# Performance work log

Hardware: AMD Instinct MI355X
Metric: run time of the kernel (lower is better)

Reference implementation:

```python
import jax, jax.numpy as jnp
import numpy as np

B, N, D, H = 2, 2048, 384, 8
Dh = D // H          # 48
G = Dh // 3          # 16 3-vectors per head
EPS = 1e-5


def setup_inputs() -> dict:
    key = jax.random.key(0)
    ks = jax.random.split(key, 8)
    x = jax.random.normal(ks[0], (B, N, D), dtype=jnp.float32)
    # per-node SE(3) frames: proper rotation matrices via QR of random Gaussians
    raw = jax.random.normal(ks[1], (B, N, 3, 3), dtype=jnp.float32)
    q, r = jnp.linalg.qr(raw)
    sign = jnp.sign(jnp.diagonal(r, axis1=-2, axis2=-1))
    frames = q * sign[..., None, :]
    s = 1.0 / np.sqrt(D)
    Wq = jax.random.normal(ks[2], (D, D), dtype=jnp.float32) * s
    Wk = jax.random.normal(ks[3], (D, D), dtype=jnp.float32) * s
    Wv = jax.random.normal(ks[4], (D, D), dtype=jnp.float32) * s
    Wo = jax.random.normal(ks[5], (D, D), dtype=jnp.float32) * s
    bo = jnp.zeros((D,), dtype=jnp.float32)
    gamma = jnp.ones((D,), dtype=jnp.float32)
    beta = jnp.zeros((D,), dtype=jnp.float32)
    return {"x": x, "frames": frames, "Wq": Wq, "Wk": Wk, "Wv": Wv,
            "Wo": Wo, "bo": bo, "gamma": gamma, "beta": beta}


def _rotate(frames, t):
    # t: [B,N,H,Dh] -> rotate each 3-vector chunk by the node's frame R_i
    b, n, h, dh = t.shape
    t3 = t.reshape(b, n, h, dh // 3, 3)
    r3 = jnp.einsum('bnij,bnhgj->bnhgi', frames, t3)
    return r3.reshape(b, n, h, dh)


def reference(x, frames, Wq, Wk, Wv, Wo, bo, gamma, beta):
    b, n, d = x.shape
    Q = (x @ Wq.T).reshape(b, n, H, Dh)
    K = (x @ Wk.T).reshape(b, n, H, Dh)
    V = (x @ Wv.T).reshape(b, n, H, Dh)
    # SE(3) frame-conditioned attention: rotate Q,K into each node's local frame
    Qr = _rotate(frames, Q)
    Kr = _rotate(frames, K)
    scores = jnp.einsum('bqhd,bkhd->bhqk', Qr, Kr) / np.sqrt(Dh)
    attn = jax.nn.softmax(scores, axis=-1)
    out = jnp.einsum('bhqk,bkhd->bqhd', attn, V).reshape(b, n, d)
    out = out @ Wo.T + bo          # out_proj; dropout is identity in eval
    y = x + out                     # residual
    mu = jnp.mean(y, axis=-1, keepdims=True)
    var = jnp.var(y, axis=-1, keepdims=True)
    return (y - mu) * jax.lax.rsqrt(var + EPS) * gamma + beta
```

## Files before the change

### kernel.cpp

```cpp
#include <hip/hip_runtime.h>
#include <hip/hip_bf16.h>
#include <math.h>

constexpr int B = 2, N = 2048, D = 384, H = 8, Dh = 48;
constexpr int M = B * N;
constexpr float EPS = 1e-5f;
constexpr int WSZ = 384 * 384;

typedef short bf16x8 __attribute__((ext_vector_type(8)));
typedef float f32x4 __attribute__((ext_vector_type(4)));

#if __has_builtin(__builtin_amdgcn_exp2f)
#define EXP2(x) __builtin_amdgcn_exp2f(x)
#else
#define EXP2(x) exp2f(x)
#endif

__device__ __forceinline__ ushort f2bf(float f) {
  union { float f; uint u; } v; v.f = f;
  uint r = v.u + 0x7fffu + ((v.u >> 16) & 1u);
  return (ushort)(r >> 16);
}
__device__ __forceinline__ float bf2f(ushort u) {
  union { uint u; float f; } v; v.u = ((uint)u) << 16;
  return v.f;
}
__device__ __forceinline__ uint pk_bf16(float lo, float hi) {
  union { __hip_bfloat162 h; uint u; } v;
  v.h = __float22bfloat162_rn(make_float2(lo, hi));
  return v.u;
}

__device__ __forceinline__ void gload16(const void* g, void* lds) {
  __builtin_amdgcn_global_load_lds(
      (const __attribute__((address_space(1))) unsigned int*)g,
      (__attribute__((address_space(3))) unsigned int*)lds, 16, 0, 0);
}

__global__ __launch_bounds__(256) void pack_all(
    const float* __restrict__ x, const float* __restrict__ Wq,
    const float* __restrict__ Wk, const float* __restrict__ Wv,
    const float* __restrict__ Wo, ushort* __restrict__ xbf,
    ushort* __restrict__ Wqkv, ushort* __restrict__ Wobf) {
  constexpr int XSZ = M * 384;
  int i = (blockIdx.x * 256 + threadIdx.x) * 8;
  const float* src; ushort* dst; int off;
  if (i < XSZ) { src = x; dst = xbf; off = i; }
  else {
    int j = i - XSZ;
    if (j < WSZ)          { src = Wq; dst = Wqkv;           off = j; }
    else if (j < 2 * WSZ) { src = Wk; dst = Wqkv + WSZ;     off = j - WSZ; }
    else if (j < 3 * WSZ) { src = Wv; dst = Wqkv + 2 * WSZ; off = j - 2 * WSZ; }
    else                  { src = Wo; dst = Wobf;           off = j - 3 * WSZ; }
  }
  float4 a = *(const float4*)(src + off);
  float4 b = *(const float4*)(src + off + 4);
  uint4 o;
  o.x = pk_bf16(a.x, a.y);
  o.y = pk_bf16(a.z, a.w);
  o.z = pk_bf16(b.x, b.y);
  o.w = pk_bf16(b.z, b.w);
  *(uint4*)(dst + off) = o;
}

__global__ __launch_bounds__(256) void gemm_qkv(
    const ushort* __restrict__ Abf, const ushort* __restrict__ Wbf,
    ushort* __restrict__ Qpad, ushort* __restrict__ Kpad,
    ushort* __restrict__ Vt) {
  __shared__ ushort Asm[64 * 32];
  __shared__ ushort Bsm[128 * 32];
  const int tid = threadIdx.x, w = tid >> 6, lane = tid & 63;
  const int lq = lane & 15, g = lane >> 4;
  const int brow = blockIdx.y * 64, bcol = blockIdx.x * 128;
  const int wr0 = (w >> 1) * 32, wc0 = (w & 1) * 64;
  const int srow = lane >> 2, scol = (lane & 3) * 8;
  f32x4 acc[2][4];
#pragma unroll
  for (int mi = 0; mi < 2; ++mi)
#pragma unroll
    for (int ni = 0; ni < 4; ++ni) acc[mi][ni] = f32x4{0.f, 0.f, 0.f, 0.f};

  for (int kt = 0; kt < 384; kt += 32) {
    __syncthreads();
    gload16(Abf + (size_t)(brow + w * 16 + srow) * 384 + kt + scol, Asm + w * 512);
#pragma unroll
    for (int i = 0; i < 2; ++i) {
      int seg = w * 2 + i;
      gload16(Wbf + (size_t)(bcol + seg * 16 + srow) * 384 + kt + scol, Bsm + seg * 512);
    }
    __syncthreads();
    bf16x8 a[2], b[4];
#pragma unroll
    for (int mi = 0; mi < 2; ++mi)
      a[mi] = *(const bf16x8*)(Asm + (wr0 + mi * 16 + lq) * 32 + g * 8);
#pragma unroll
    for (int ni = 0; ni < 4; ++ni)
      b[ni] = *(const bf16x8*)(Bsm + (wc0 + ni * 16 + lq) * 32 + g * 8);
#pragma unroll
    for (int mi = 0; mi < 2; ++mi)
#pragma unroll
      for (int ni = 0; ni < 4; ++ni)
        acc[mi][ni] = __builtin_amdgcn_mfma_f32_16x16x32_bf16(a[mi], b[ni], acc[mi][ni], 0, 0, 0);
  }

  if (bcol < 768) {
#pragma unroll
    for (int mi = 0; mi < 2; ++mi)
#pragma unroll
      for (int ni = 0; ni < 4; ++ni) {
        int colD = bcol + wc0 + ni * 16 + lq;
        ushort* dstm = (colD < 384) ? Qpad : Kpad;
        int c = (colD < 384) ? colD : colD - 384;
        int hh = c / 48, dh = c - hh * 48;
#pragma unroll
        for (int r = 0; r < 4; ++r) {
          int row = brow + wr0 + mi * 16 + g * 4 + r;
          dstm[(size_t)row * 512 + hh * 64 + dh] = f2bf(acc[mi][ni][r]);
        }
      }
  } else {
#pragma unroll
    for (int mi = 0; mi < 2; ++mi)
#pragma unroll
      for (int ni = 0; ni < 4; ++ni) {
        int vcol = bcol + wc0 + ni * 16 + lq - 768;
        int hh = vcol / 48, dh = vcol - hh * 48;
#pragma unroll
        for (int r = 0; r < 4; ++r) {
          int row = brow + wr0 + mi * 16 + g * 4 + r;
          int bb = row >> 11, nn = row & 2047;
          Vt[((size_t)(bb * H + hh) * 48 + dh) * N + nn] = f2bf(acc[mi][ni][r]);
        }
      }
  }
}

__global__ __launch_bounds__(256) void rotate_both(
    ushort* __restrict__ Q, ushort* __restrict__ K,
    const float* __restrict__ F, float qscale) {
  constexpr int TOT = M * H * 16;
  int idx = blockIdx.x * 256 + threadIdx.x;
  ushort* T = (idx < TOT) ? Q : K;
  float scale = (idx < TOT) ? qscale : 1.0f;
  int rem = (idx < TOT) ? idx : idx - TOT;
  int gq = rem & 15;
  int nh = rem >> 4;
  int h = nh & 7;
  int bn = nh >> 3;
  ushort* p = T + (size_t)bn * 512 + h * 64;
  if (gq < 8) *(uint*)(p + 48 + gq * 2) = 0u;
  ushort* s = p + gq * 3;
  const float* R = F + (size_t)bn * 9;
  float v0 = bf2f(s[0]), v1 = bf2f(s[1]), v2 = bf2f(s[2]);
  float w0 = (R[0] * v0 + R[1] * v1 + R[2] * v2) * scale;
  float w1 = (R[3] * v0 + R[4] * v1 + R[5] * v2) * scale;
  float w2 = (R[6] * v0 + R[7] * v1 + R[8] * v2) * scale;
  s[0] = f2bf(w0); s[1] = f2bf(w1); s[2] = f2bf(w2);
}

__global__ __launch_bounds__(128) void attn_mfma(
    const ushort* __restrict__ Qpad, const ushort* __restrict__ Kpad,
    const ushort* __restrict__ Vt, ushort* __restrict__ Pacc,
    float* __restrict__ Pml) {
  __shared__ __align__(16) ushort SH[14336];
  ushort* K0 = SH;
  ushort* K1 = SH + 4096;
  ushort* V0 = SH + 8192;
  ushort* V1 = SH + 11264;

  const int bid = blockIdx.x;
  const int wg = (bid & 7) * 128 + (bid >> 3);
  const int qt = wg & 31;
  const int rest = wg >> 5;
  const int h = rest & 7;
  const int b = (rest >> 3) & 1;
  const int half = rest >> 4;
  const int kt0 = half * 1024;
  const int tid = threadIdx.x;
  const int w = tid >> 6;
  const int lane = tid & 63;
  const int lq = lane & 15;
  const int g = lane >> 4;
  const int l7 = lq & 7;
  const int srow8 = lane >> 3;
  const int c8 = (lane & 7) ^ srow8;

  bf16x8 qf[2][2];
  {
    const ushort* qb = Qpad + ((size_t)(b * N) + qt * 64 + w * 32) * 512 + h * 64;
#pragma unroll
    for (int i = 0; i < 2; ++i)
#pragma unroll
      for (int kd = 0; kd < 2; ++kd)
        qf[i][kd] = *(const bf16x8*)(qb + (size_t)(i * 16 + lq) * 512 + kd * 32 + g * 8);
  }

  const ushort* kg[4];
#pragma unroll
  for (int j = 0; j < 4; ++j) {
    int s = w + 2 * j;
    int kappa = (s >> 2) * 32 + (s & 1) * 16 + (srow8 >> 2) * 8 + ((s >> 1) & 1) * 4 + (srow8 & 3);
    kg[j] = Kpad + ((size_t)(b * N) + kt0 + kappa) * 512 + h * 64 + c8 * 8;
  }
  const ushort* vg[3];
#pragma unroll
  for (int j = 0; j < 3; ++j) {
    int sv = w + 2 * j;
    vg[j] = Vt + ((size_t)(b * H + h) * 48 + sv * 8 + srow8) * (size_t)N + kt0 + c8 * 8;
  }

  auto stage = [&](ushort* kb, ushort* vb) {
#pragma unroll
    for (int j = 0; j < 4; ++j) {
      gload16(kg[j], kb + (w + 2 * j) * 512);
      kg[j] += 64 * 512;
    }
#pragma unroll
    for (int j = 0; j < 3; ++j) {
      gload16(vg[j], vb + (w + 2 * j) * 512);
      vg[j] += 64;
    }
  };

  float m[2] = {-3.0e38f, -3.0e38f}, l[2] = {0.f, 0.f};
  f32x4 oacc[2][3];
#pragma unroll
  for (int i = 0; i < 2; ++i)
#pragma unroll
    for (int d = 0; d < 3; ++d) oacc[i][d] = f32x4{0.f, 0.f, 0.f, 0.f};

  stage(K0, V0);
  __syncthreads();
  int cur = 0;

  for (int t = 0; t < 16; ++t) {
    if (t < 15) stage(cur ? K0 : K1, cur ? V0 : V1);
    const ushort* Kc = cur ? K1 : K0;
    const ushort* Vc = cur ? V1 : V0;

    f32x4 st[2][4];
#pragma unroll
    for (int i = 0; i < 2; ++i)
#pragma unroll
      for (int t4 = 0; t4 < 4; ++t4) st[i][t4] = f32x4{0.f, 0.f, 0.f, 0.f};
#pragma unroll
    for (int t4 = 0; t4 < 4; ++t4) {
      bf16x8 a0 = *(const bf16x8*)(Kc + (t4 * 16 + lq) * 64 + ((g ^ l7) * 8));
      bf16x8 a1 = *(const bf16x8*)(Kc + (t4 * 16 + lq) * 64 + (((g + 4) ^ l7) * 8));
#pragma unroll
      for (int i = 0; i < 2; ++i) {
        st[i][t4] = __builtin_amdgcn_mfma_f32_16x16x32_bf16(a0, qf[i][0], st[i][t4], 0, 0, 0);
        st[i][t4] = __builtin_amdgcn_mfma_f32_16x16x32_bf16(a1, qf[i][1], st[i][t4], 0, 0, 0);
      }
    }

    bf16x8 vf[2][3];
#pragma unroll
    for (int ks = 0; ks < 2; ++ks)
#pragma unroll
      for (int d = 0; d < 3; ++d)
        vf[ks][d] = *(const bf16x8*)(Vc + (d * 16 + lq) * 64 + ((((ks << 2) | g) ^ l7) * 8));

    float tmax[2];
#pragma unroll
    for (int i = 0; i < 2; ++i) {
      float t0 = st[i][0][0];
#pragma unroll
      for (int t4 = 0; t4 < 4; ++t4)
#pragma unroll
        for (int r = 0; r < 4; ++r) t0 = fmaxf(t0, st[i][t4][r]);
      t0 = fmaxf(t0, __shfl_xor(t0, 16));
      t0 = fmaxf(t0, __shfl_xor(t0, 32));
      tmax[i] = t0;
    }
    bool need = (tmax[0] > m[0] + 8.0f) | (tmax[1] > m[1] + 8.0f);
    if (__ballot(need)) {
#pragma unroll
      for (int i = 0; i < 2; ++i) {
        float mnew = fmaxf(m[i], tmax[i]);
        float corr = EXP2(m[i] - mnew);
        m[i] = mnew;
        l[i] *= corr;
#pragma unroll
        for (int r = 0; r < 4; ++r) {
          float cr = __shfl(corr, g * 4 + r);
#pragma unroll
          for (int d = 0; d < 3; ++d) oacc[i][d][r] *= cr;
        }
      }
    }

    bf16x8 pf[2][2];
#pragma unroll
    for (int i = 0; i < 2; ++i) {
      float ps = 0.f;
      uint u0[4], u1[4];
#pragma unroll
      for (int t4 = 0; t4 < 4; ++t4) {
        float p0 = EXP2(st[i][t4][0] - m[i]);
        float p1 = EXP2(st[i][t4][1] - m[i]);
        float p2 = EXP2(st[i][t4][2] - m[i]);
        float p3 = EXP2(st[i][t4][3] - m[i]);
        ps += (p0 + p1) + (p2 + p3);
        if (t4 < 2) {
          u0[(t4 & 1) * 2]     = pk_bf16(p0, p1);
          u0[(t4 & 1) * 2 + 1] = pk_bf16(p2, p3);
        } else {
          u1[(t4 & 1) * 2]     = pk_bf16(p0, p1);
          u1[(t4 & 1) * 2 + 1] = pk_bf16(p2, p3);
        }
      }
      ps += __shfl_xor(ps, 16);
      ps += __shfl_xor(ps, 32);
      l[i] += ps;
      union { uint4 q; bf16x8 v; } c0, c1;
      c0.q = make_uint4(u0[0], u0[1], u0[2], u0[3]);
      c1.q = make_uint4(u1[0], u1[1], u1[2], u1[3]);
      pf[i][0] = c0.v;
      pf[i][1] = c1.v;
    }

#pragma unroll
    for (int ks = 0; ks < 2; ++ks)
#pragma unroll
      for (int i = 0; i < 2; ++i)
#pragma unroll
        for (int d = 0; d < 3; ++d)
          oacc[i][d] = __builtin_amdgcn_mfma_f32_16x16x32_bf16(pf[i][ks], vf[ks][d], oacc[i][d], 0, 0, 0);

    __syncthreads();
    cur ^= 1;
  }

#pragma unroll
  for (int i = 0; i < 2; ++i) {
    const size_t pr0 = ((size_t)((half * B + b) * H + h)) * N + qt * 64 + (w * 2 + i) * 16;
#pragma unroll
    for (int d = 0; d < 3; ++d)
#pragma unroll
      for (int r = 0; r < 4; ++r)
        Pacc[(pr0 + g * 4 + r) * 48 + d * 16 + lq] = f2bf(oacc[i][d][r]);
    if (g == 0) {
      Pml[(pr0 + lq) * 2] = m[i];
      Pml[(pr0 + lq) * 2 + 1] = l[i];
    }
  }
}

__global__ __launch_bounds__(256) void attn_merge(
    const ushort* __restrict__ Pacc, const float* __restrict__ Pml,
    ushort* __restrict__ Obf) {
  int idx = blockIdx.x * 256 + threadIdx.x;
  int h = idx & 7, bn = idx >> 3;
  int b = bn >> 11, n = bn & 2047;
  size_t r0 = ((size_t)(b * H + h)) * N + n;
  size_t r1 = ((size_t)((B + b) * H + h)) * N + n;
  float m0 = Pml[r0 * 2], l0 = Pml[r0 * 2 + 1];
  float m1 = Pml[r1 * 2], l1 = Pml[r1 * 2 + 1];
  float mm = fmaxf(m0, m1);
  float w0 = EXP2(m0 - mm), w1 = EXP2(m1 - mm);
  float inv = 1.f / (l0 * w0 + l1 * w1);
  w0 *= inv; w1 *= inv;
  const ushort* p0 = Pacc + r0 * 48;
  const ushort* p1 = Pacc + r1 * 48;
  ushort* ob = Obf + (size_t)bn * 384 + h * 48;
#pragma unroll
  for (int j = 0; j < 6; ++j) {
    uint4 a = *(const uint4*)(p0 + j * 8);
    uint4 c = *(const uint4*)(p1 + j * 8);
    uint4 o;
    o.x = pk_bf16(bf2f((ushort)a.x) * w0 + bf2f((ushort)c.x) * w1,
                  bf2f((ushort)(a.x >> 16)) * w0 + bf2f((ushort)(c.x >> 16)) * w1);
    o.y = pk_bf16(bf2f((ushort)a.y) * w0 + bf2f((ushort)c.y) * w1,
                  bf2f((ushort)(a.y >> 16)) * w0 + bf2f((ushort)(c.y >> 16)) * w1);
    o.z = pk_bf16(bf2f((ushort)a.z) * w0 + bf2f((ushort)c.z) * w1,
                  bf2f((ushort)(a.z >> 16)) * w0 + bf2f((ushort)(c.z >> 16)) * w1);
    o.w = pk_bf16(bf2f((ushort)a.w) * w0 + bf2f((ushort)c.w) * w1,
                  bf2f((ushort)(a.w >> 16)) * w0 + bf2f((ushort)(c.w >> 16)) * w1);
    *(uint4*)(ob + j * 8) = o;
  }
}

__global__ __launch_bounds__(256) void gemm_out_ln(
    const ushort* __restrict__ Abf, const ushort* __restrict__ Wbf,
    const float* __restrict__ x, const float* __restrict__ bo,
    const float* __restrict__ gamma, const float* __restrict__ beta,
    float* __restrict__ out) {
  __shared__ ushort Asm[16 * 32];
  __shared__ ushort Bsm[384 * 32];
  __shared__ float red[4][16][2];
  const int tid = threadIdx.x, w = tid >> 6, lane = tid & 63;
  const int lq = lane & 15, g = lane >> 4;
  const int brow = blockIdx.x * 16;
  const int srow = lane >> 2, scol = (lane & 3) * 8;
  f32x4 acc[6];
#pragma unroll
  for (int ni = 0; ni < 6; ++ni) acc[ni] = f32x4{0.f, 0.f, 0.f, 0.f};

  for (int kt = 0; kt < 384; kt += 32) {
    __syncthreads();
    if (w == 0) gload16(Abf + (size_t)(brow + srow) * 384 + kt + scol, Asm);
#pragma unroll
    for (int i = 0; i < 6; ++i) {
      int seg = w * 6 + i;
      gload16(Wbf + (size_t)(seg * 16 + srow) * 384 + kt + scol, Bsm + seg * 512);
    }
    __syncthreads();
    bf16x8 a = *(const bf16x8*)(Asm + lq * 32 + g * 8);
#pragma unroll
    for (int ni = 0; ni < 6; ++ni) {
      bf16x8 bb = *(const bf16x8*)(Bsm + ((w * 6 + ni) * 16 + lq) * 32 + g * 8);
      acc[ni] = __builtin_amdgcn_mfma_f32_16x16x32_bf16(a, bb, acc[ni], 0, 0, 0);
    }
  }

  float s[4] = {0.f, 0.f, 0.f, 0.f}, s2[4] = {0.f, 0.f, 0.f, 0.f};
#pragma unroll
  for (int ni = 0; ni < 6; ++ni) {
    int col = (w * 6 + ni) * 16 + lq;
    float bcol = bo[col];
#pragma unroll
    for (int r = 0; r < 4; ++r) {
      float y = acc[ni][r] + x[(size_t)(brow + g * 4 + r) * 384 + col] + bcol;
      acc[ni][r] = y;
      s[r] += y; s2[r] += y * y;
    }
  }
#pragma unroll
  for (int o = 1; o < 16; o <<= 1) {
#pragma unroll
    for (int r = 0; r < 4; ++r) {
      s[r] += __shfl_xor(s[r], o);
      s2[r] += __shfl_xor(s2[r], o);
    }
  }
  if (lq == 0) {
#pragma unroll
    for (int r = 0; r < 4; ++r) {
      red[w][g * 4 + r][0] = s[r];
      red[w][g * 4 + r][1] = s2[r];
    }
  }
  __syncthreads();
#pragma unroll
  for (int r = 0; r < 4; ++r) {
    int row = g * 4 + r;
    float ts  = red[0][row][0] + red[1][row][0] + red[2][row][0] + red[3][row][0];
    float ts2 = red[0][row][1] + red[1][row][1] + red[2][row][1] + red[3][row][1];
    float mu = ts * (1.f / 384.f);
    float var = ts2 * (1.f / 384.f) - mu * mu;
    float rstd = rsqrtf(var + EPS);
    float* orow = out + (size_t)(brow + row) * 384;
#pragma unroll
    for (int ni = 0; ni < 6; ++ni) {
      int col = (w * 6 + ni) * 16 + lq;
      orow[col] = (acc[ni][r] - mu) * rstd * gamma[col] + beta[col];
    }
  }
}

extern "C" void kernel_launch(void* const* d_in, const int* in_sizes, int n_in,
                              void* d_out, int out_size, void* d_ws, size_t ws_size,
                              hipStream_t stream) {
  const float* x      = (const float*)d_in[0];
  const float* frames = (const float*)d_in[1];
  const float* Wq     = (const float*)d_in[2];
  const float* Wk     = (const float*)d_in[3];
  const float* Wv     = (const float*)d_in[4];
  const float* Wo     = (const float*)d_in[5];
  const float* bo     = (const float*)d_in[6];
  const float* gamma  = (const float*)d_in[7];
  const float* beta   = (const float*)d_in[8];
  float* out = (float*)d_out;

  ushort* xbf  = (ushort*)d_ws;
  ushort* Obf  = xbf;
  ushort* Wqkv = xbf + (size_t)M * 384;
  ushort* Wobf = Wqkv + 3 * (size_t)WSZ;
  ushort* Qpad = Wobf + (size_t)WSZ;
  ushort* Kpad = Qpad + (size_t)M * 512;
  ushort* Vt   = Kpad + (size_t)M * 512;
  ushort* Pacc = Vt + (size_t)M * 384;
  float*  Pml  = (float*)(Pacc + (size_t)2 * B * H * N * 48);

  const float qscale = 0.14433756729740643f * 1.4426950408889634f;

  pack_all<<<(M * 384 + 4 * WSZ) / (8 * 256), 256, 0, stream>>>(
      x, Wq, Wk, Wv, Wo, xbf, Wqkv, Wobf);

  gemm_qkv<<<dim3(9, 64), 256, 0, stream>>>(xbf, Wqkv, Qpad, Kpad, Vt);

  rotate_both<<<2 * M * H * 16 / 256, 256, 0, stream>>>(Qpad, Kpad, frames, qscale);

  attn_mfma<<<2 * B * H * (N / 64), 128, 0, stream>>>(Qpad, Kpad, Vt, Pacc, Pml);

  attn_merge<<<M * H / 256, 256, 0, stream>>>(Pacc, Pml, Obf);

  gemm_out_ln<<<M / 16, 256, 0, stream>>>(Obf, Wobf, x, bo, gamma, beta, out);
}
```

Baseline: 78.42 us.

## Fuse attention merge into out-proj GEMM, widen attention blocks, vectorize rotation

The split-K attention merge kernel is removed. Its rescale of the two partial outputs by their max and sum weights now happens while gemm_out_ln loads A tiles into shared memory, which saves one launch and the Obf round trip through global memory. The attention kernel now runs 256 threads per block over 128 query rows, so each K/V tile staged in shared memory is reused by four waves instead of two. rotate_both now handles a whole head row per thread with 16-byte loads and stores instead of one 3-vector per thread. The trade-off is extra address math and merge work inside the GEMM's A-load path, done by a single wave.

```diff
diff --git a/kernel.cpp b/kernel.cpp
--- a/kernel.cpp
+++ b/kernel.cpp
@@ -138,27 +138,46 @@
 __global__ __launch_bounds__(256) void rotate_both(
     ushort* __restrict__ Q, ushort* __restrict__ K,
     const float* __restrict__ F, float qscale) {
-  constexpr int TOT = M * H * 16;
   int idx = blockIdx.x * 256 + threadIdx.x;
-  ushort* T = (idx < TOT) ? Q : K;
-  float scale = (idx < TOT) ? qscale : 1.0f;
-  int rem = (idx < TOT) ? idx : idx - TOT;
-  int gq = rem & 15;
-  int nh = rem >> 4;
-  int h = nh & 7;
-  int bn = nh >> 3;
-  ushort* p = T + (size_t)bn * 512 + h * 64;
-  if (gq < 8) *(uint*)(p + 48 + gq * 2) = 0u;
-  ushort* s = p + gq * 3;
+  int h = idx & 7;
+  int bn = (idx >> 3) & 4095;
+  int mat = idx >> 15;
+  ushort* p = (mat ? K : Q) + (size_t)bn * 512 + h * 64;
+  float scale = mat ? 1.0f : qscale;
   const float* R = F + (size_t)bn * 9;
-  float v0 = bf2f(s[0]), v1 = bf2f(s[1]), v2 = bf2f(s[2]);
-  float w0 = (R[0] * v0 + R[1] * v1 + R[2] * v2) * scale;
-  float w1 = (R[3] * v0 + R[4] * v1 + R[5] * v2) * scale;
-  float w2 = (R[6] * v0 + R[7] * v1 + R[8] * v2) * scale;
-  s[0] = f2bf(w0); s[1] = f2bf(w1); s[2] = f2bf(w2);
-}
-
-__global__ __launch_bounds__(128) void attn_mfma(
+  float r0 = R[0], r1 = R[1], r2 = R[2];
+  float r3 = R[3], r4 = R[4], r5 = R[5];
+  float r6 = R[6], r7 = R[7], r8 = R[8];
+  uint u[24];
+#pragma unroll
+  for (int j = 0; j < 6; ++j)
+    *(uint4*)(u + j * 4) = *(const uint4*)(p + j * 8);
+  float f[48];
+#pragma unroll
+  for (int j = 0; j < 24; ++j) {
+    f[2 * j] = bf2f((ushort)u[j]);
+    f[2 * j + 1] = bf2f((ushort)(u[j] >> 16));
+  }
+  float o[48];
+#pragma unroll
+  for (int t = 0; t < 16; ++t) {
+    float v0 = f[3 * t], v1 = f[3 * t + 1], v2 = f[3 * t + 2];
+    o[3 * t]     = (r0 * v0 + r1 * v1 + r2 * v2) * scale;
+    o[3 * t + 1] = (r3 * v0 + r4 * v1 + r5 * v2) * scale;
+    o[3 * t + 2] = (r6 * v0 + r7 * v1 + r8 * v2) * scale;
+  }
+  uint ow[24];
+#pragma unroll
+  for (int j = 0; j < 24; ++j) ow[j] = pk_bf16(o[2 * j], o[2 * j + 1]);
+#pragma unroll
+  for (int j = 0; j < 6; ++j)
+    *(uint4*)(p + j * 8) = *(uint4*)(ow + j * 4);
+  uint4 z = make_uint4(0, 0, 0, 0);
+  *(uint4*)(p + 48) = z;
+  *(uint4*)(p + 56) = z;
+}
+
+__global__ __launch_bounds__(256) void attn_mfma(
     const ushort* __restrict__ Qpad, const ushort* __restrict__ Kpad,
     const ushort* __restrict__ Vt, ushort* __restrict__ Pacc,
     float* __restrict__ Pml) {
@@ -169,9 +188,9 @@
   ushort* V1 = SH + 11264;
 
   const int bid = blockIdx.x;
-  const int wg = (bid & 7) * 128 + (bid >> 3);
-  const int qt = wg & 31;
-  const int rest = wg >> 5;
+  const int wg = (bid & 7) * 64 + (bid >> 3);
+  const int qt = wg & 15;
+  const int rest = wg >> 4;
   const int h = rest & 7;
   const int b = (rest >> 3) & 1;
   const int half = rest >> 4;
@@ -187,7 +206,7 @@
 
   bf16x8 qf[2][2];
   {
-    const ushort* qb = Qpad + ((size_t)(b * N) + qt * 64 + w * 32) * 512 + h * 64;
+    const ushort* qb = Qpad + ((size_t)(b * N) + qt * 128 + w * 32) * 512 + h * 64;
 #pragma unroll
     for (int i = 0; i < 2; ++i)
 #pragma unroll
@@ -195,31 +214,25 @@
         qf[i][kd] = *(const bf16x8*)(qb + (size_t)(i * 16 + lq) * 512 + kd * 32 + g * 8);
   }
 
-  const ushort* kg[4];
-#pragma unroll
-  for (int j = 0; j < 4; ++j) {
-    int s = w + 2 * j;
-    int kappa = (s >> 2) * 32 + (s & 1) * 16 + (srow8 >> 2) * 8 + ((s >> 1) & 1) * 4 + (srow8 & 3);
-    kg[j] = Kpad + ((size_t)(b * N) + kt0 + kappa) * 512 + h * 64 + c8 * 8;
-  }
-  const ushort* vg[3];
-#pragma unroll
-  for (int j = 0; j < 3; ++j) {
-    int sv = w + 2 * j;
-    vg[j] = Vt + ((size_t)(b * H + h) * 48 + sv * 8 + srow8) * (size_t)N + kt0 + c8 * 8;
-  }
+  const ushort* kg0;
+  const ushort* kg1;
+  {
+    int s0 = w;
+    int k0i = (s0 >> 2) * 32 + (s0 & 1) * 16 + (srow8 >> 2) * 8 + ((s0 >> 1) & 1) * 4 + (srow8 & 3);
+    kg0 = Kpad + ((size_t)(b * N) + kt0 + k0i) * 512 + h * 64 + c8 * 8;
+    int s1 = w + 4;
+    int k1i = (s1 >> 2) * 32 + (s1 & 1) * 16 + (srow8 >> 2) * 8 + ((s1 >> 1) & 1) * 4 + (srow8 & 3);
+    kg1 = Kpad + ((size_t)(b * N) + kt0 + k1i) * 512 + h * 64 + c8 * 8;
+  }
+  const ushort* vg0 = Vt + ((size_t)(b * H + h) * 48 + w * 8 + srow8) * (size_t)N + kt0 + c8 * 8;
+  const ushort* vg1 = vg0 + 32 * (size_t)N;
 
   auto stage = [&](ushort* kb, ushort* vb) {
-#pragma unroll
-    for (int j = 0; j < 4; ++j) {
-      gload16(kg[j], kb + (w + 2 * j) * 512);
-      kg[j] += 64 * 512;
-    }
-#pragma unroll
-    for (int j = 0; j < 3; ++j) {
-      gload16(vg[j], vb + (w + 2 * j) * 512);
-      vg[j] += 64;
-    }
+    gload16(kg0, kb + w * 512);
+    gload16(kg1, kb + (w + 4) * 512);
+    gload16(vg0, vb + w * 512);
+    if (w < 2) gload16(vg1, vb + (w + 4) * 512);
+    kg0 += 64 * 512; kg1 += 64 * 512; vg0 += 64; vg1 += 64;
   };
 
   float m[2] = {-3.0e38f, -3.0e38f}, l[2] = {0.f, 0.f};
@@ -334,7 +347,7 @@
 
 #pragma unroll
   for (int i = 0; i < 2; ++i) {
-    const size_t pr0 = ((size_t)((half * B + b) * H + h)) * N + qt * 64 + (w * 2 + i) * 16;
+    const size_t pr0 = ((size_t)((half * B + b) * H + h)) * N + qt * 128 + w * 32 + i * 16;
 #pragma unroll
     for (int d = 0; d < 3; ++d)
 #pragma unroll
@@ -347,59 +360,61 @@
   }
 }
 
-__global__ __launch_bounds__(256) void attn_merge(
+__global__ __launch_bounds__(256) void gemm_out_ln(
     const ushort* __restrict__ Pacc, const float* __restrict__ Pml,
-    ushort* __restrict__ Obf) {
-  int idx = blockIdx.x * 256 + threadIdx.x;
-  int h = idx & 7, bn = idx >> 3;
-  int b = bn >> 11, n = bn & 2047;
-  size_t r0 = ((size_t)(b * H + h)) * N + n;
-  size_t r1 = ((size_t)((B + b) * H + h)) * N + n;
-  float m0 = Pml[r0 * 2], l0 = Pml[r0 * 2 + 1];
-  float m1 = Pml[r1 * 2], l1 = Pml[r1 * 2 + 1];
-  float mm = fmaxf(m0, m1);
-  float w0 = EXP2(m0 - mm), w1 = EXP2(m1 - mm);
-  float inv = 1.f / (l0 * w0 + l1 * w1);
-  w0 *= inv; w1 *= inv;
-  const ushort* p0 = Pacc + r0 * 48;
-  const ushort* p1 = Pacc + r1 * 48;
-  ushort* ob = Obf + (size_t)bn * 384 + h * 48;
-#pragma unroll
-  for (int j = 0; j < 6; ++j) {
-    uint4 a = *(const uint4*)(p0 + j * 8);
-    uint4 c = *(const uint4*)(p1 + j * 8);
-    uint4 o;
-    o.x = pk_bf16(bf2f((ushort)a.x) * w0 + bf2f((ushort)c.x) * w1,
-                  bf2f((ushort)(a.x >> 16)) * w0 + bf2f((ushort)(c.x >> 16)) * w1);
-    o.y = pk_bf16(bf2f((ushort)a.y) * w0 + bf2f((ushort)c.y) * w1,
-                  bf2f((ushort)(a.y >> 16)) * w0 + bf2f((ushort)(c.y >> 16)) * w1);
-    o.z = pk_bf16(bf2f((ushort)a.z) * w0 + bf2f((ushort)c.z) * w1,
-                  bf2f((ushort)(a.z >> 16)) * w0 + bf2f((ushort)(c.z >> 16)) * w1);
-    o.w = pk_bf16(bf2f((ushort)a.w) * w0 + bf2f((ushort)c.w) * w1,
-                  bf2f((ushort)(a.w >> 16)) * w0 + bf2f((ushort)(c.w >> 16)) * w1);
-    *(uint4*)(ob + j * 8) = o;
-  }
-}
-
-__global__ __launch_bounds__(256) void gemm_out_ln(
-    const ushort* __restrict__ Abf, const ushort* __restrict__ Wbf,
-    const float* __restrict__ x, const float* __restrict__ bo,
-    const float* __restrict__ gamma, const float* __restrict__ beta,
-    float* __restrict__ out) {
+    const ushort* __restrict__ Wbf, const float* __restrict__ x,
+    const float* __restrict__ bo, const float* __restrict__ gamma,
+    const float* __restrict__ beta, float* __restrict__ out) {
   __shared__ ushort Asm[16 * 32];
   __shared__ ushort Bsm[384 * 32];
   __shared__ float red[4][16][2];
+  __shared__ float Wm[16][8][2];
   const int tid = threadIdx.x, w = tid >> 6, lane = tid & 63;
   const int lq = lane & 15, g = lane >> 4;
   const int brow = blockIdx.x * 16;
   const int srow = lane >> 2, scol = (lane & 3) * 8;
+
+  if (tid < 128) {
+    int r = tid >> 3, hh = tid & 7;
+    int gr = brow + r;
+    int bb = gr >> 11, nn = gr & 2047;
+    size_t i0 = ((size_t)(bb * H + hh)) * N + nn;
+    size_t i1 = ((size_t)((B + bb) * H + hh)) * N + nn;
+    float m0 = Pml[i0 * 2], l0 = Pml[i0 * 2 + 1];
+    float m1 = Pml[i1 * 2], l1 = Pml[i1 * 2 + 1];
+    float mm = fmaxf(m0, m1);
+    float e0 = EXP2(m0 - mm), e1 = EXP2(m1 - mm);
+    float inv = 1.f / (l0 * e0 + l1 * e1);
+    Wm[r][hh][0] = e0 * inv;
+    Wm[r][hh][1] = e1 * inv;
+  }
+  __syncthreads();
+
   f32x4 acc[6];
 #pragma unroll
   for (int ni = 0; ni < 6; ++ni) acc[ni] = f32x4{0.f, 0.f, 0.f, 0.f};
 
   for (int kt = 0; kt < 384; kt += 32) {
     __syncthreads();
-    if (w == 0) gload16(Abf + (size_t)(brow + srow) * 384 + kt + scol, Asm);
+    if (w == 0) {
+      int col = kt + scol;
+      int hh = col / 48;
+      int dcol = col - hh * 48;
+      int gr = brow + srow;
+      int bb = gr >> 11, nn = gr & 2047;
+      const ushort* a0p = Pacc + (((size_t)(bb * H + hh)) * N + nn) * 48 + dcol;
+      const ushort* a1p = Pacc + (((size_t)((B + bb) * H + hh)) * N + nn) * 48 + dcol;
+      bf16x8 a0 = *(const bf16x8*)a0p;
+      bf16x8 a1 = *(const bf16x8*)a1p;
+      float w0v = Wm[srow][hh][0], w1v = Wm[srow][hh][1];
+      uint mg[4];
+#pragma unroll
+      for (int j = 0; j < 4; ++j)
+        mg[j] = pk_bf16(
+            bf2f((ushort)a0[2 * j]) * w0v + bf2f((ushort)a1[2 * j]) * w1v,
+            bf2f((ushort)a0[2 * j + 1]) * w0v + bf2f((ushort)a1[2 * j + 1]) * w1v);
+      *(uint4*)(Asm + srow * 32 + scol) = make_uint4(mg[0], mg[1], mg[2], mg[3]);
+    }
 #pragma unroll
     for (int i = 0; i < 6; ++i) {
       int seg = w * 6 + i;
@@ -409,8 +424,8 @@
     bf16x8 a = *(const bf16x8*)(Asm + lq * 32 + g * 8);
 #pragma unroll
     for (int ni = 0; ni < 6; ++ni) {
-      bf16x8 bb = *(const bf16x8*)(Bsm + ((w * 6 + ni) * 16 + lq) * 32 + g * 8);
-      acc[ni] = __builtin_amdgcn_mfma_f32_16x16x32_bf16(a, bb, acc[ni], 0, 0, 0);
+      bf16x8 bb2 = *(const bf16x8*)(Bsm + ((w * 6 + ni) * 16 + lq) * 32 + g * 8);
+      acc[ni] = __builtin_amdgcn_mfma_f32_16x16x32_bf16(a, bb2, acc[ni], 0, 0, 0);
     }
   }
 
@@ -474,7 +489,6 @@
   float* out = (float*)d_out;
 
   ushort* xbf  = (ushort*)d_ws;
-  ushort* Obf  = xbf;
   ushort* Wqkv = xbf + (size_t)M * 384;
   ushort* Wobf = Wqkv + 3 * (size_t)WSZ;
   ushort* Qpad = Wobf + (size_t)WSZ;
@@ -490,11 +504,9 @@
 
   gemm_qkv<<<dim3(9, 64), 256, 0, stream>>>(xbf, Wqkv, Qpad, Kpad, Vt);
 
-  rotate_both<<<2 * M * H * 16 / 256, 256, 0, stream>>>(Qpad, Kpad, frames, qscale);
-
-  attn_mfma<<<2 * B * H * (N / 64), 128, 0, stream>>>(Qpad, Kpad, Vt, Pacc, Pml);
-
-  attn_merge<<<M * H / 256, 256, 0, stream>>>(Pacc, Pml, Obf);
-
-  gemm_out_ln<<<M / 16, 256, 0, stream>>>(Obf, Wobf, x, bo, gamma, beta, out);
-}
+  rotate_both<<<2 * M * H / 256, 256, 0, stream>>>(Qpad, Kpad, frames, qscale);
+
+  attn_mfma<<<2 * B * H * (N / 128), 256, 0, stream>>>(Qpad, Kpad, Vt, Pacc, Pml);
+
+  gemm_out_ln<<<M / 16, 256, 0, stream>>>(Pacc, Pml, Wobf, x, bo, gamma, beta, out);
+}
```

After: 74.67 us. 4.8% less time.
